# Kernel optimization log

Measured on AMD Instinct MI355X. Metric: run time of the kernel, lower is better.

## Reference

```python
import jax, jax.numpy as jnp
import numpy as np

B, LQ, LK, D, H = 4, 2048, 2048, 768, 12
DH = D // H  # 64
EPS = 1e-5


def setup_inputs() -> dict:
    key = jax.random.key(0)
    ks = jax.random.split(key, 12)
    s = 0.02
    return {
        "queries": jax.random.normal(ks[0], (B, LQ, D), jnp.float32),
        "keys": jax.random.normal(ks[1], (B, LK, D), jnp.float32),
        "values": jax.random.normal(ks[2], (B, LK, D), jnp.float32),
        "mask": jax.random.randint(ks[3], (B, LK), 0, 2, jnp.int32),
        "Wq": jax.random.normal(ks[4], (D, D), jnp.float32) * s,
        "Wk": jax.random.normal(ks[5], (D, D), jnp.float32) * s,
        "Wv": jax.random.normal(ks[6], (D, D), jnp.float32) * s,
        "Wo": jax.random.normal(ks[7], (D, D), jnp.float32) * s,
        "W1": jax.random.normal(ks[8], (D, D), jnp.float32) * s,
        "b1": jnp.zeros((D,), jnp.float32),
        "W2": jax.random.normal(ks[9], (D, D), jnp.float32) * s,
        "b2": jnp.zeros((D,), jnp.float32),
        "ln_g": jnp.ones((D,), jnp.float32),
        "ln_b": jnp.zeros((D,), jnp.float32),
    }


def _split_heads(x):
    # [B, L, D] -> [B, H, L, DH]
    b, l, _ = x.shape
    return x.reshape(b, l, H, DH).transpose(0, 2, 1, 3)


def reference(queries, keys, values, mask, Wq, Wk, Wv, Wo, W1, b1, W2, b2, ln_g, ln_b):
    q = _split_heads(queries @ Wq)  # [B,H,LQ,DH]
    k = _split_heads(keys @ Wk)     # [B,H,LK,DH]
    v = _split_heads(values @ Wv)   # [B,H,LK,DH]

    scores = jnp.einsum("bhqd,bhkd->bhqk", q, k) / jnp.sqrt(jnp.float32(DH))

    # valid length per batch row = count of nonzero mask entries; positions >= valid_len are masked
    valid_lens = jnp.sum(mask != 0, axis=1)  # [B]
    key_ok = jnp.arange(LK, dtype=jnp.int32)[None, :] < valid_lens[:, None]  # [B,LK]
    scores = jnp.where(key_ok[:, None, None, :], scores, jnp.float32(-1e6))

    attn = jax.nn.softmax(scores, axis=-1)  # dropout is identity in eval
    out = jnp.einsum("bhqk,bhkd->bhqd", attn, v)  # [B,H,LQ,DH]
    out = out.transpose(0, 2, 1, 3).reshape(out.shape[0], out.shape[2], D)

    att_out = out @ Wo  # [B,LQ,D]
    ffn = jax.nn.relu(att_out @ W1 + b1) @ W2 + b2

    # residual + layernorm (torch code intends ln(dropout(ffn) + att_out))
    y = ffn + att_out
    mu = jnp.mean(y, axis=-1, keepdims=True)
    var = jnp.mean(jnp.square(y - mu), axis=-1, keepdims=True)
    return (y - mu) / jnp.sqrt(var + EPS) * ln_g + ln_b
```

## Files before the change

### kernel.cpp

```cpp
#include <hip/hip_runtime.h>
#include <stdint.h>

typedef __attribute__((ext_vector_type(4))) float floatx4;
typedef __attribute__((ext_vector_type(8))) __bf16 bf16x8;
typedef __attribute__((ext_vector_type(4))) __bf16 bf16x4;

#define DEV __device__ __forceinline__

constexpr int HB = 12;
constexpr int LSEQ = 2048;
constexpr int DMODEL = 768;
constexpr int MROWS = 8192;
constexpr float QSCALE = 0.125f * 1.44269504088896f;

DEV short f2bf(float f) {
  union { float f; uint32_t u; } x; x.f = f;
  uint32_t r = x.u + 0x7FFFu + ((x.u >> 16) & 1u);
  return (short)(r >> 16);
}

DEV float bf2f(short s) {
  union { uint32_t u; float f; } x; x.u = ((uint32_t)(uint16_t)s) << 16;
  return x.f;
}

typedef __attribute__((address_space(1))) void as1_void;
typedef __attribute__((address_space(3))) void as3_void;

DEV void gload_lds16(const void* g, void* l) {
  __builtin_amdgcn_global_load_lds((as1_void*)(uintptr_t)g, (as3_void*)l, 16, 0, 0);
}

__global__ __launch_bounds__(256)
void transpose_k(const float* w0, const float* w1, const float* w2,
                 const float* w3, const float* w4, const float* w5,
                 short* o0, short* o1, short* o2, short* o3, short* o4, short* o5)
{
  const float* W; short* O;
  switch (blockIdx.z) {
    case 0: W = w0; O = o0; break;
    case 1: W = w1; O = o1; break;
    case 2: W = w2; O = o2; break;
    case 3: W = w3; O = o3; break;
    case 4: W = w4; O = o4; break;
    default: W = w5; O = o5; break;
  }
  __shared__ float t[32][33];
  const int tx = threadIdx.x & 31, ty = threadIdx.x >> 5;
  const int n0 = blockIdx.x * 32, k0 = blockIdx.y * 32;
#pragma unroll
  for (int i = 0; i < 4; ++i)
    t[ty + i * 8][tx] = W[(size_t)(k0 + ty + i * 8) * DMODEL + n0 + tx];
  __syncthreads();
#pragma unroll
  for (int i = 0; i < 4; ++i)
    O[(size_t)(n0 + ty + i * 8) * DMODEL + k0 + tx] = f2bf(t[tx][ty + i * 8]);
}

__global__ __launch_bounds__(256)
void cvt_k(const float* __restrict__ s0, const float* __restrict__ s1, const float* __restrict__ s2,
           short* __restrict__ d0, short* __restrict__ d1, short* __restrict__ d2)
{
  const float* s; short* d;
  switch (blockIdx.y) { case 0: s = s0; d = d0; break; case 1: s = s1; d = d1; break; default: s = s2; d = d2; break; }
  const size_t i = ((size_t)blockIdx.x * 256 + threadIdx.x) * 4;
  const float4 v = *(const float4*)(s + i);
  short4 r; r.x = f2bf(v.x); r.y = f2bf(v.y); r.z = f2bf(v.z); r.w = f2bf(v.w);
  *(short4*)(d + i) = r;
}

__global__ __launch_bounds__(256)
void vlens_k(const int* __restrict__ mask, int* __restrict__ vl)
{
  const int b = blockIdx.x;
  int s = 0;
  for (int i = threadIdx.x; i < LSEQ; i += 256) s += (mask[b * LSEQ + i] != 0) ? 1 : 0;
#pragma unroll
  for (int o = 32; o >= 1; o >>= 1) s += __shfl_xor(s, o);
  __shared__ int red[4];
  const int lane = threadIdx.x & 63, wave = threadIdx.x >> 6;
  if (lane == 0) red[wave] = s;
  __syncthreads();
  if (threadIdx.x == 0) vl[b] = red[0] + red[1] + red[2] + red[3];
}

enum { EPI_QKV = 0, EPI_PLAIN = 2, EPI_BIAS_RELU = 3, EPI_Y = 4 };

template <int EPI>
__global__ __launch_bounds__(256)
void gemm_k(const short* __restrict__ A0, const short* __restrict__ A1, const short* __restrict__ A2,
            const short* __restrict__ B0, const short* __restrict__ B1, const short* __restrict__ B2,
            const float* __restrict__ bias, const short* __restrict__ resid,
            void* __restrict__ o0, void* __restrict__ o1, void* __restrict__ o2)
{
  __shared__ __align__(16) short As[2][64 * 32];
  __shared__ __align__(16) short Bs[2][128 * 32];
  const short* A = A0;
  const short* Bt = B0;
  if constexpr (EPI == EPI_QKV) {
    if (blockIdx.z == 1) { A = A1; Bt = B1; }
    else if (blockIdx.z == 2) { A = A2; Bt = B2; }
  }
  const int tid = threadIdx.x;
  const int lane = tid & 63, wave = tid >> 6;
  const int wm = wave >> 1, wn = wave & 1;
  const int m0 = blockIdx.y * 64, n0 = blockIdx.x * 128;
  const int col = lane & 15, quad = lane >> 4;
  const int sr = lane >> 2;
  const int sk = (lane & 3) * 8;

  floatx4 acc[2][4] = {};

  for (int kt = 0; kt < 12; ++kt) {
    const int k0 = kt * 64;
    __syncthreads();
#pragma unroll
    for (int h = 0; h < 2; ++h) {
      gload_lds16(A + (size_t)(m0 + wave * 16 + sr) * DMODEL + k0 + h * 32 + sk, As[h] + wave * 512);
#pragma unroll
      for (int c = 0; c < 2; ++c) {
        const int ch = wave * 2 + c;
        gload_lds16(Bt + (size_t)(n0 + ch * 16 + sr) * DMODEL + k0 + h * 32 + sk, Bs[h] + ch * 512);
      }
    }
    __syncthreads();
#pragma unroll
    for (int h = 0; h < 2; ++h) {
      bf16x8 af[2], bfr[4];
#pragma unroll
      for (int t = 0; t < 2; ++t)
        af[t] = *(const bf16x8*)&As[h][(wm * 32 + t * 16 + col) * 32 + quad * 8];
#pragma unroll
      for (int t = 0; t < 4; ++t)
        bfr[t] = *(const bf16x8*)&Bs[h][(wn * 64 + t * 16 + col) * 32 + quad * 8];
#pragma unroll
      for (int mt = 0; mt < 2; ++mt)
#pragma unroll
        for (int nt = 0; nt < 4; ++nt)
          acc[mt][nt] = __builtin_amdgcn_mfma_f32_16x16x32_bf16(af[mt], bfr[nt], acc[mt][nt], 0, 0, 0);
    }
  }

#pragma unroll
  for (int mt = 0; mt < 2; ++mt) {
#pragma unroll
    for (int nt = 0; nt < 4; ++nt) {
#pragma unroll
      for (int r = 0; r < 4; ++r) {
        const int m = m0 + wm * 32 + mt * 16 + quad * 4 + r;
        const int n = n0 + wn * 64 + nt * 16 + col;
        float v = acc[mt][nt][r];
        if constexpr (EPI == EPI_QKV) {
          const int b = m >> 11, l = m & 2047, h = n >> 6, dh = n & 63;
          const int z = blockIdx.z;
          if (z == 0) {
            ((short*)o0)[((size_t)(b * HB + h) * LSEQ + l) * 64 + dh] = f2bf(v * QSCALE);
          } else if (z == 1) {
            ((short*)o1)[((size_t)(b * HB + h) * LSEQ + l) * 64 + dh] = f2bf(v);
          } else {
            ((short*)o2)[((size_t)(b * HB + h) * 64 + dh) * LSEQ + l] = f2bf(v);
          }
        } else if constexpr (EPI == EPI_PLAIN) {
          ((short*)o0)[(size_t)m * DMODEL + n] = f2bf(v);
        } else if constexpr (EPI == EPI_BIAS_RELU) {
          v += bias[n]; v = v > 0.f ? v : 0.f;
          ((short*)o0)[(size_t)m * DMODEL + n] = f2bf(v);
        } else {
          v += bias[n] + bf2f(resid[(size_t)m * DMODEL + n]);
          ((float*)o0)[(size_t)m * DMODEL + n] = v;
        }
      }
    }
  }
}

constexpr int PSP = 68;
__global__ __launch_bounds__(256)
void attn_k(const short* __restrict__ qw, const short* __restrict__ kw, const short* __restrict__ vtw,
            const int* __restrict__ vlens, short* __restrict__ outp)
{
  __shared__ __align__(16) short Qs[2][128][32];
  __shared__ __align__(16) short Ks[2][64][32];
  __shared__ __align__(16) short Vts[2][64][32];
  __shared__ __align__(16) short Ps[4][32 * PSP];

  const int tid = threadIdx.x;
  const int lane = tid & 63, wave = tid >> 6;
  const int col = lane & 15, quad = lane >> 4;
  const int bh = blockIdx.y, b = bh / HB, h = bh % HB;
  const int q0 = blockIdx.x * 128;
  const int vl = vlens[b];
  const int sr = lane >> 2, sk = (lane & 3) * 8;

  const short* qbase = qw  + (size_t)bh * LSEQ * 64;
  const short* kbase = kw  + (size_t)bh * LSEQ * 64;
  const short* vbase = vtw + (size_t)bh * 64 * LSEQ;

#pragma unroll
  for (int i = 0; i < 4; ++i) {
    const int c = wave * 4 + i;
    const int hs = c >> 3, r0 = (c & 7) * 16;
    gload_lds16(qbase + (size_t)(q0 + r0 + sr) * 64 + hs * 32 + sk, &Qs[hs][r0][0]);
  }

  floatx4 oacc[2][4] = {};
  float li[2][4] = {};

  const int ktend = (vl > 0) ? ((vl + 63) >> 6) : (LSEQ / 64);

  for (int kt = 0; kt < ktend; ++kt) {
    __syncthreads();
#pragma unroll
    for (int i = 0; i < 2; ++i) {
      const int c = wave * 2 + i;
      const int hs = c >> 2, r0 = (c & 3) * 16;
      gload_lds16(kbase + (size_t)(kt * 64 + r0 + sr) * 64 + hs * 32 + sk, &Ks[hs][r0][0]);
      gload_lds16(vbase + (size_t)(r0 + sr) * LSEQ + kt * 64 + hs * 32 + sk, &Vts[hs][r0][0]);
    }
    __syncthreads();

    floatx4 sacc[2][4] = {};
#pragma unroll
    for (int ks = 0; ks < 2; ++ks) {
      bf16x8 aq[2], bk[4];
#pragma unroll
      for (int mt = 0; mt < 2; ++mt)
        aq[mt] = *(const bf16x8*)&Qs[ks][wave * 32 + mt * 16 + col][quad * 8];
#pragma unroll
      for (int nt = 0; nt < 4; ++nt)
        bk[nt] = *(const bf16x8*)&Ks[ks][nt * 16 + col][quad * 8];
#pragma unroll
      for (int mt = 0; mt < 2; ++mt)
#pragma unroll
        for (int nt = 0; nt < 4; ++nt)
          sacc[mt][nt] = __builtin_amdgcn_mfma_f32_16x16x32_bf16(aq[mt], bk[nt], sacc[mt][nt], 0, 0, 0);
    }

    if (kt * 64 + 64 > vl) {
#pragma unroll
      for (int nt = 0; nt < 4; ++nt) {
        const bool ok = (kt * 64 + nt * 16 + col) < vl;
#pragma unroll
        for (int mt = 0; mt < 2; ++mt)
#pragma unroll
          for (int r = 0; r < 4; ++r)
            sacc[mt][nt][r] = ok ? sacc[mt][nt][r] : -1.0e6f;
      }
    }

#pragma unroll
    for (int mt = 0; mt < 2; ++mt)
#pragma unroll
      for (int nt = 0; nt < 4; ++nt)
#pragma unroll
        for (int r = 0; r < 4; ++r) {
          const float p = __builtin_amdgcn_exp2f(sacc[mt][nt][r]);
          li[mt][r] += p;
          union { float f; uint32_t u; } pu; pu.f = p;
          Ps[wave][(mt * 16 + quad * 4 + r) * PSP + nt * 16 + col] =
              (short)((pu.u + 0x8000u) >> 16);
        }

    asm volatile("s_waitcnt lgkmcnt(0)" ::: "memory");

#pragma unroll
    for (int ks = 0; ks < 2; ++ks) {
      bf16x8 ap[2], bv[4];
#pragma unroll
      for (int mt = 0; mt < 2; ++mt) {
        union { bf16x8 v8; bf16x4 v4[2]; } u;
        const short* base = &Ps[wave][(mt * 16 + col) * PSP + ks * 32 + quad * 8];
        u.v4[0] = *(const bf16x4*)base;
        u.v4[1] = *(const bf16x4*)(base + 4);
        ap[mt] = u.v8;
      }
#pragma unroll
      for (int nt = 0; nt < 4; ++nt)
        bv[nt] = *(const bf16x8*)&Vts[ks][nt * 16 + col][quad * 8];
#pragma unroll
      for (int mt = 0; mt < 2; ++mt)
#pragma unroll
        for (int nt = 0; nt < 4; ++nt)
          oacc[mt][nt] = __builtin_amdgcn_mfma_f32_16x16x32_bf16(ap[mt], bv[nt], oacc[mt][nt], 0, 0, 0);
    }
  }

  float rli[2][4];
#pragma unroll
  for (int mt = 0; mt < 2; ++mt)
#pragma unroll
    for (int r = 0; r < 4; ++r) {
      float t = li[mt][r];
      t += __shfl_xor(t, 1); t += __shfl_xor(t, 2);
      t += __shfl_xor(t, 4); t += __shfl_xor(t, 8);
      rli[mt][r] = 1.0f / fmaxf(t, 1e-30f);
    }

#pragma unroll
  for (int mt = 0; mt < 2; ++mt)
#pragma unroll
    for (int nt = 0; nt < 4; ++nt)
#pragma unroll
      for (int r = 0; r < 4; ++r) {
        const int qrow = q0 + wave * 32 + mt * 16 + quad * 4 + r;
        const int dh = nt * 16 + col;
        const float v = oacc[mt][nt][r] * rli[mt][r];
        outp[((size_t)b * LSEQ + qrow) * DMODEL + h * 64 + dh] = f2bf(v);
      }
}

__global__ __launch_bounds__(256)
void ln_k(const float* __restrict__ y, const float* __restrict__ g, const float* __restrict__ be,
          float* __restrict__ o)
{
  const int row = blockIdx.x;
  const int tid = threadIdx.x;
  const float* yr = y + (size_t)row * DMODEL;
  float v[3];
  float s = 0.f, sq = 0.f;
#pragma unroll
  for (int i = 0; i < 3; ++i) { v[i] = yr[tid + i * 256]; s += v[i]; sq += v[i] * v[i]; }
#pragma unroll
  for (int off = 32; off >= 1; off >>= 1) { s += __shfl_xor(s, off); sq += __shfl_xor(sq, off); }
  __shared__ float red[8];
  const int lane = tid & 63, wave = tid >> 6;
  if (lane == 0) { red[wave] = s; red[4 + wave] = sq; }
  __syncthreads();
  s = red[0] + red[1] + red[2] + red[3];
  sq = red[4] + red[5] + red[6] + red[7];
  const float mu = s * (1.f / 768.f);
  const float var = sq * (1.f / 768.f) - mu * mu;
  const float rstd = rsqrtf(var + 1e-5f);
  float* orow = o + (size_t)row * DMODEL;
#pragma unroll
  for (int i = 0; i < 3; ++i) {
    const int c = tid + i * 256;
    orow[c] = (v[i] - mu) * rstd * g[c] + be[c];
  }
}

extern "C" void kernel_launch(void* const* d_in, const int* in_sizes, int n_in,
                              void* d_out, int out_size, void* d_ws, size_t ws_size,
                              hipStream_t stream)
{
  const float* queries = (const float*)d_in[0];
  const float* keys    = (const float*)d_in[1];
  const float* values  = (const float*)d_in[2];
  const int*   mask    = (const int*)d_in[3];
  const float* Wq = (const float*)d_in[4];
  const float* Wk = (const float*)d_in[5];
  const float* Wv = (const float*)d_in[6];
  const float* Wo = (const float*)d_in[7];
  const float* W1 = (const float*)d_in[8];
  const float* b1 = (const float*)d_in[9];
  const float* W2 = (const float*)d_in[10];
  const float* b2 = (const float*)d_in[11];
  const float* ln_g = (const float*)d_in[12];
  const float* ln_b = (const float*)d_in[13];

  char* ws = (char*)d_ws;
  size_t off = 0;
  auto alloc = [&](size_t bytes) -> void* {
    void* p = ws + off;
    off = (off + bytes + 255) & ~(size_t)255;
    return p;
  };
  int* vlens = (int*)alloc(256);
  short* wt[6];
  for (int i = 0; i < 6; ++i) wt[i] = (short*)alloc((size_t)DMODEL * DMODEL * 2);
  constexpr size_t SB = (size_t)MROWS * DMODEL * 2;
  short* xq  = (short*)alloc(SB);
  short* xk  = (short*)alloc(SB);
  short* xv  = (short*)alloc(SB);
  short* qw  = (short*)alloc(SB);
  short* kw  = (short*)alloc(SB);
  short* vtw = (short*)alloc(SB);
  short* attn_cat = xq;
  short* atto_bf  = xk;
  short* h1       = xv;
  float* yb       = (float*)qw;

  dim3 blk(256);
  transpose_k<<<dim3(24, 24, 6), blk, 0, stream>>>(Wq, Wk, Wv, Wo, W1, W2,
                                                   wt[0], wt[1], wt[2], wt[3], wt[4], wt[5]);
  cvt_k<<<dim3(6144, 3), blk, 0, stream>>>(queries, keys, values, xq, xk, xv);
  vlens_k<<<dim3(4), blk, 0, stream>>>(mask, vlens);
  gemm_k<EPI_QKV><<<dim3(6, 128, 3), blk, 0, stream>>>(
      xq, xk, xv, wt[0], wt[1], wt[2], nullptr, nullptr, qw, kw, vtw);
  attn_k<<<dim3(16, 48), blk, 0, stream>>>(qw, kw, vtw, vlens, attn_cat);
  gemm_k<EPI_PLAIN><<<dim3(6, 128, 1), blk, 0, stream>>>(
      attn_cat, nullptr, nullptr, wt[3], nullptr, nullptr, nullptr, nullptr,
      atto_bf, nullptr, nullptr);
  gemm_k<EPI_BIAS_RELU><<<dim3(6, 128, 1), blk, 0, stream>>>(
      atto_bf, nullptr, nullptr, wt[4], nullptr, nullptr, b1, nullptr,
      h1, nullptr, nullptr);
  gemm_k<EPI_Y><<<dim3(6, 128, 1), blk, 0, stream>>>(
      h1, nullptr, nullptr, wt[5], nullptr, nullptr, b2, atto_bf,
      yb, nullptr, nullptr);
  ln_k<<<dim3(MROWS), blk, 0, stream>>>(yb, ln_g, ln_b, (float*)d_out);
}
```

Baseline: 349.1 us.

## Double-buffer GEMM LDS tiles and swap grid axes for block ordering

The GEMM kernel now uses two LDS buffers and issues the global-to-LDS loads for the next K tile before computing the current one. It replaces the two __syncthreads per iteration with raw s_barrier plus an s_waitcnt vmcnt(6) that lets the prefetched loads stay in flight. Separately, the grid axes of the GEMM and attention launches are swapped so consecutive blocks walk along M (or along heads) instead of N (or query tiles), which changes which blocks share cache. The change doubles GEMM LDS use and depends on the hand-written waitcnt count matching the number of loads issued per stage.

```diff
diff --git a/kernel.cpp b/kernel.cpp
--- a/kernel.cpp
+++ b/kernel.cpp
@@ -93,8 +93,8 @@
             const float* __restrict__ bias, const short* __restrict__ resid,
             void* __restrict__ o0, void* __restrict__ o1, void* __restrict__ o2)
 {
-  __shared__ __align__(16) short As[2][64 * 32];
-  __shared__ __align__(16) short Bs[2][128 * 32];
+  __shared__ __align__(16) short As[2][2][64 * 32];
+  __shared__ __align__(16) short Bs[2][2][128 * 32];
   const short* A = A0;
   const short* Bt = B0;
   if constexpr (EPI == EPI_QKV) {
@@ -104,35 +104,47 @@
   const int tid = threadIdx.x;
   const int lane = tid & 63, wave = tid >> 6;
   const int wm = wave >> 1, wn = wave & 1;
-  const int m0 = blockIdx.y * 64, n0 = blockIdx.x * 128;
+  const int m0 = blockIdx.x * 64, n0 = blockIdx.y * 128;
   const int col = lane & 15, quad = lane >> 4;
   const int sr = lane >> 2;
   const int sk = (lane & 3) * 8;
 
+  const short* Arow = A + (size_t)(m0 + wave * 16 + sr) * DMODEL + sk;
+  const short* Brow0 = Bt + (size_t)(n0 + (wave * 2 + 0) * 16 + sr) * DMODEL + sk;
+  const short* Brow1 = Bt + (size_t)(n0 + (wave * 2 + 1) * 16 + sr) * DMODEL + sk;
+
+  auto stage = [&](int kt, int buf) {
+    const int k0 = kt * 64;
+#pragma unroll
+    for (int h = 0; h < 2; ++h) {
+      gload_lds16(Arow + k0 + h * 32, &As[buf][h][wave * 512]);
+      gload_lds16(Brow0 + k0 + h * 32, &Bs[buf][h][(wave * 2 + 0) * 512]);
+      gload_lds16(Brow1 + k0 + h * 32, &Bs[buf][h][(wave * 2 + 1) * 512]);
+    }
+  };
+
   floatx4 acc[2][4] = {};
 
+  stage(0, 0);
   for (int kt = 0; kt < 12; ++kt) {
-    const int k0 = kt * 64;
-    __syncthreads();
-#pragma unroll
-    for (int h = 0; h < 2; ++h) {
-      gload_lds16(A + (size_t)(m0 + wave * 16 + sr) * DMODEL + k0 + h * 32 + sk, As[h] + wave * 512);
-#pragma unroll
-      for (int c = 0; c < 2; ++c) {
-        const int ch = wave * 2 + c;
-        gload_lds16(Bt + (size_t)(n0 + ch * 16 + sr) * DMODEL + k0 + h * 32 + sk, Bs[h] + ch * 512);
-      }
-    }
-    __syncthreads();
+    const int cur = kt & 1;
+    asm volatile("s_barrier" ::: "memory");
+    if (kt + 1 < 12) {
+      stage(kt + 1, cur ^ 1);
+      asm volatile("s_waitcnt vmcnt(6)" ::: "memory");
+    } else {
+      asm volatile("s_waitcnt vmcnt(0)" ::: "memory");
+    }
+    asm volatile("s_barrier" ::: "memory");
 #pragma unroll
     for (int h = 0; h < 2; ++h) {
       bf16x8 af[2], bfr[4];
 #pragma unroll
       for (int t = 0; t < 2; ++t)
-        af[t] = *(const bf16x8*)&As[h][(wm * 32 + t * 16 + col) * 32 + quad * 8];
+        af[t] = *(const bf16x8*)&As[cur][h][(wm * 32 + t * 16 + col) * 32 + quad * 8];
 #pragma unroll
       for (int t = 0; t < 4; ++t)
-        bfr[t] = *(const bf16x8*)&Bs[h][(wn * 64 + t * 16 + col) * 32 + quad * 8];
+        bfr[t] = *(const bf16x8*)&Bs[cur][h][(wn * 64 + t * 16 + col) * 32 + quad * 8];
 #pragma unroll
       for (int mt = 0; mt < 2; ++mt)
 #pragma unroll
@@ -187,8 +199,8 @@
   const int tid = threadIdx.x;
   const int lane = tid & 63, wave = tid >> 6;
   const int col = lane & 15, quad = lane >> 4;
-  const int bh = blockIdx.y, b = bh / HB, h = bh % HB;
-  const int q0 = blockIdx.x * 128;
+  const int bh = blockIdx.x, b = bh / HB, h = bh % HB;
+  const int q0 = blockIdx.y * 128;
   const int vl = vlens[b];
   const int sr = lane >> 2, sk = (lane & 3) * 8;
 
@@ -385,16 +397,16 @@
                                                    wt[0], wt[1], wt[2], wt[3], wt[4], wt[5]);
   cvt_k<<<dim3(6144, 3), blk, 0, stream>>>(queries, keys, values, xq, xk, xv);
   vlens_k<<<dim3(4), blk, 0, stream>>>(mask, vlens);
-  gemm_k<EPI_QKV><<<dim3(6, 128, 3), blk, 0, stream>>>(
+  gemm_k<EPI_QKV><<<dim3(128, 6, 3), blk, 0, stream>>>(
       xq, xk, xv, wt[0], wt[1], wt[2], nullptr, nullptr, qw, kw, vtw);
-  attn_k<<<dim3(16, 48), blk, 0, stream>>>(qw, kw, vtw, vlens, attn_cat);
-  gemm_k<EPI_PLAIN><<<dim3(6, 128, 1), blk, 0, stream>>>(
+  attn_k<<<dim3(48, 16), blk, 0, stream>>>(qw, kw, vtw, vlens, attn_cat);
+  gemm_k<EPI_PLAIN><<<dim3(128, 6, 1), blk, 0, stream>>>(
       attn_cat, nullptr, nullptr, wt[3], nullptr, nullptr, nullptr, nullptr,
       atto_bf, nullptr, nullptr);
-  gemm_k<EPI_BIAS_RELU><<<dim3(6, 128, 1), blk, 0, stream>>>(
+  gemm_k<EPI_BIAS_RELU><<<dim3(128, 6, 1), blk, 0, stream>>>(
       atto_bf, nullptr, nullptr, wt[4], nullptr, nullptr, b1, nullptr,
       h1, nullptr, nullptr);
-  gemm_k<EPI_Y><<<dim3(6, 128, 1), blk, 0, stream>>>(
+  gemm_k<EPI_Y><<<dim3(128, 6, 1), blk, 0, stream>>>(
       h1, nullptr, nullptr, wt[5], nullptr, nullptr, b2, atto_bf,
       yb, nullptr, nullptr);
   ln_k<<<dim3(MROWS), blk, 0, stream>>>(yb, ln_g, ln_b, (float*)d_out);
```

After: 332.6 us. 1.05x faster.
